# Kernel optimization log

Measured on AMD Instinct MI355X. Metric: run time of the kernel, lower is better.

The kernel has to match this reference:

```python
import jax, jax.numpy as jnp
import numpy as np

DIM = 384
H_RES, W_RES = 56, 56
HEADS = 12
WS = 7          # window size
SS = 3          # shift size
N = WS * WS     # tokens per window
NW = (H_RES // WS) * (W_RES // WS)
EPS = 1e-5


def _rel_pos_index(ws):
    coords = np.stack(np.meshgrid(np.arange(ws), np.arange(ws), indexing='ij'))  # [2,ws,ws]
    cf = coords.reshape(2, -1)                      # [2, N]
    rc = (cf[:, :, None] - cf[:, None, :]).transpose(1, 2, 0)  # [N,N,2]
    rc[..., 0] += ws - 1
    rc[..., 1] += ws - 1
    rc[..., 0] *= 2 * ws - 1
    return rc.sum(-1)                               # [N,N] int


def _attn_mask(h, w, ws, ss):
    img = np.zeros((h, w))
    cnt = 0
    slices = (slice(0, -ws), slice(-ws, -ss), slice(-ss, None))
    for hs in slices:
        for wsl in slices:
            img[hs, wsl] = cnt
            cnt += 1
    mw = img.reshape(h // ws, ws, w // ws, ws).transpose(0, 2, 1, 3).reshape(-1, ws * ws)  # [nW,N]
    d = mw[:, None, :] - mw[:, :, None]
    return np.where(d != 0, -100.0, 0.0).astype(np.float32)  # [nW,N,N]


RPI = jnp.asarray(_rel_pos_index(WS).reshape(-1))          # [N*N]
ATTN_MASK = jnp.asarray(_attn_mask(H_RES, W_RES, WS, SS))  # [nW,N,N]


def _layernorm(x, g, b):
    mu = jnp.mean(x, axis=-1, keepdims=True)
    var = jnp.mean(jnp.square(x - mu), axis=-1, keepdims=True)
    return (x - mu) * jax.lax.rsqrt(var + EPS) * g + b


def setup_inputs() -> dict:
    key = jax.random.key(0)
    ks = jax.random.split(key, 8)
    s = 0.02
    return {
        'x': jax.random.normal(ks[0], (32, 1 + H_RES * W_RES, DIM), jnp.float32),
        'norm1_g': jnp.ones((DIM,), jnp.float32),
        'norm1_b': jnp.zeros((DIM,), jnp.float32),
        'qkv_w': jax.random.normal(ks[1], (DIM, 3 * DIM), jnp.float32) * s,
        'qkv_b': jnp.zeros((3 * DIM,), jnp.float32),
        'rpb_table': jax.random.normal(ks[2], ((2 * WS - 1) ** 2, HEADS), jnp.float32) * s,
        'proj_w': jax.random.normal(ks[3], (DIM, DIM), jnp.float32) * s,
        'proj_b': jnp.zeros((DIM,), jnp.float32),
        'norm2_g': jnp.ones((DIM,), jnp.float32),
        'norm2_b': jnp.zeros((DIM,), jnp.float32),
        'fc1_w': jax.random.normal(ks[4], (DIM, 4 * DIM), jnp.float32) * s,
        'fc1_b': jnp.zeros((4 * DIM,), jnp.float32),
        'fc2_w': jax.random.normal(ks[5], (4 * DIM, DIM), jnp.float32) * s,
        'fc2_b': jnp.zeros((DIM,), jnp.float32),
    }


def reference(x, norm1_g, norm1_b, qkv_w, qkv_b, rpb_table, proj_w, proj_b,
              norm2_g, norm2_b, fc1_w, fc1_b, fc2_w, fc2_b):
    B = x.shape[0]
    C = DIM
    hd = C // HEADS
    scale = hd ** -0.5

    time_token = x[:, :1, :]          # [B,1,C]
    img = x[:, 1:, :]                 # [B,H*W,C]
    shortcut = img

    h = _layernorm(img, norm1_g, norm1_b).reshape(B, H_RES, W_RES, C)
    h = jnp.roll(h, shift=(-SS, -SS), axis=(1, 2))  # cyclic shift

    # window partition -> [B*nW, N, C]
    xw = h.reshape(B, H_RES // WS, WS, W_RES // WS, WS, C)
    xw = xw.transpose(0, 1, 3, 2, 4, 5).reshape(-1, N, C)

    # window attention
    qkv = (xw @ qkv_w + qkv_b).reshape(-1, N, 3, HEADS, hd).transpose(2, 0, 3, 1, 4)
    q, k, v = qkv[0], qkv[1], qkv[2]                 # [B*nW, H, N, hd]
    attn = jnp.einsum('whnd,whmd->whnm', q * scale, k)
    bias = rpb_table[RPI].reshape(N, N, HEADS).transpose(2, 0, 1)  # [H,N,N]
    attn = attn + bias[None]
    attn = attn.reshape(B, NW, HEADS, N, N) + ATTN_MASK[None, :, None]
    attn = jax.nn.softmax(attn.reshape(-1, HEADS, N, N), axis=-1)
    out = jnp.einsum('whnm,whmd->wnhd', attn, v).reshape(-1, N, C)
    out = out @ proj_w + proj_b

    # window reverse -> [B,H,W,C]
    out = out.reshape(B, H_RES // WS, W_RES // WS, WS, WS, C)
    out = out.transpose(0, 1, 3, 2, 4, 5).reshape(B, H_RES, W_RES, C)
    out = jnp.roll(out, shift=(SS, SS), axis=(1, 2)).reshape(B, H_RES * W_RES, C)

    img = shortcut + out
    x = jnp.concatenate([time_token, img], axis=1)   # [B,1+H*W,C]
    x = _layernorm(x, norm2_g, norm2_b)
    hmlp = jax.nn.gelu(x @ fc1_w + fc1_b, approximate=False)
    x = x + (hmlp @ fc2_w + fc2_b)
    return x
```

## Files before the change

### kernel.cpp

```cpp
#include <hip/hip_runtime.h>
#include <hip/hip_bf16.h>

#define DIM 384
#define HEADS 12
#define NTOK 49
#define TOKENS 3137
#define M_ATTN 100352
#define M_FULL 100384
#define M_PAD  100480
#define SCALEQ 0.17677669529663687f

typedef __attribute__((ext_vector_type(8))) short s8v;
typedef __attribute__((ext_vector_type(4))) float f4v;
typedef unsigned short u16;

__device__ __forceinline__ float b2f(int s) {
  union { unsigned u; float f; } c; c.u = ((unsigned)(s & 0xffff)) << 16; return c.f;
}
__device__ __forceinline__ u16 f2b(float f) {
  __hip_bfloat16 h = __float2bfloat16(f);
  return *reinterpret_cast<u16*>(&h);
}
__device__ __forceinline__ void gload16(const void* g, void* l) {
  __builtin_amdgcn_global_load_lds((const __attribute__((address_space(1))) void*)g,
                                   (__attribute__((address_space(3))) void*)l, 16, 0, 0);
}

__global__ void k_convert(const float* __restrict__ qkv_w, const float* __restrict__ qkv_b,
                          const float* __restrict__ proj_w, const float* __restrict__ fc1_w,
                          const float* __restrict__ fc2_w,
                          u16* __restrict__ wt_qkv, float* __restrict__ qkvb_s,
                          u16* __restrict__ wt_proj, u16* __restrict__ wt_fc1,
                          u16* __restrict__ wt_fc2) {
  int i = blockIdx.x * 256 + threadIdx.x;
  if (i < 1152 * 384) { int n = i / 384, k = i % 384;
    float v = qkv_w[(size_t)k * 1152 + n]; if (n < 384) v *= SCALEQ; wt_qkv[i] = f2b(v); }
  if (i < 1152) qkvb_s[i] = qkv_b[i] * (i < 384 ? SCALEQ : 1.0f);
  if (i < 384 * 384) { int n = i / 384, k = i % 384; wt_proj[i] = f2b(proj_w[(size_t)k * 384 + n]); }
  if (i < 1536 * 384) { int n = i / 384, k = i % 384; wt_fc1[i] = f2b(fc1_w[(size_t)k * 1536 + n]); }
  if (i < 384 * 1536) { int n = i / 1536, k = i % 1536; wt_fc2[i] = f2b(fc2_w[(size_t)k * 384 + n]); }
}

__global__ void k_addtab(const float* __restrict__ rpb, float* __restrict__ ADD) {
  int idx = blockIdx.x * 256 + threadIdx.x;
  if (idx >= 4 * HEADS * NTOK * NTOK) return;
  int j = idx % NTOK, t = idx / NTOK;
  int i = t % NTOK; t /= NTOK;
  int h = t % HEADS; int cls = t / HEADS;
  int ii = i / 7, jj = i % 7, ji = j / 7, j2 = j % 7;
  int rpi = (ii - ji + 6) * 13 + (jj - j2 + 6);
  float v = rpb[rpi * HEADS + h];
  int rh = (cls & 2) ? (ii < 4 ? 1 : 2) : 0;
  int rw = (cls & 1) ? (jj < 4 ? 1 : 2) : 0;
  int sh = (cls & 2) ? (ji < 4 ? 1 : 2) : 0;
  int sw = (cls & 1) ? (j2 < 4 ? 1 : 2) : 0;
  if (rh != sh || rw != sw) v -= 100.0f;
  ADD[idx] = v;
}

__global__ void k_ln1(const float* __restrict__ x, const float* __restrict__ g,
                      const float* __restrict__ b, u16* __restrict__ xw, int t0) {
  int wid = threadIdx.x >> 6, lane = threadIdx.x & 63;
  int t = t0 + blockIdx.x * 4 + wid;
  int bi = t / 3136, rem = t % 3136;
  int win = rem / NTOK, n = rem % NTOK;
  int wh = win >> 3, ww = win & 7, ii = n / 7, jj = n % 7;
  int h = (wh * 7 + ii + 3) % 56;
  int w = (ww * 7 + jj + 3) % 56;
  const float* src = x + ((size_t)bi * TOKENS + 1 + h * 56 + w) * DIM;
  float v[6];
  #pragma unroll
  for (int e = 0; e < 6; e++) v[e] = src[lane + e * 64];
  float s = v[0] + v[1] + v[2] + v[3] + v[4] + v[5];
  #pragma unroll
  for (int m = 1; m < 64; m <<= 1) s += __shfl_xor(s, m);
  float mu = s * (1.0f / 384.0f);
  float q = 0.f;
  #pragma unroll
  for (int e = 0; e < 6; e++) { float d = v[e] - mu; q += d * d; }
  #pragma unroll
  for (int m = 1; m < 64; m <<= 1) q += __shfl_xor(q, m);
  float rstd = rsqrtf(q * (1.0f / 384.0f) + 1e-5f);
  u16* dst = xw + (size_t)(t - t0) * DIM;
  #pragma unroll
  for (int e = 0; e < 6; e++) {
    int c = lane + e * 64;
    dst[c] = f2b((v[e] - mu) * rstd * g[c] + b[c]);
  }
}

template<int MODE>
__global__ __launch_bounds__(256) void k_gemm(
    const u16* __restrict__ A, const u16* __restrict__ Bt,
    const float* __restrict__ bias, u16* __restrict__ Cb,
    float* __restrict__ outp, const u16* __restrict__ resid,
    int N, int K, int row_off) {
  __shared__ __align__(16) u16 As[2][128 * 64];
  __shared__ __align__(16) u16 Bs[2][128 * 64];
  int gx = gridDim.x;
  int lid = blockIdx.y * gx + blockIdx.x;
  int nwg = gx * gridDim.y;
  int q = nwg >> 3, r = nwg & 7;
  int xcd = lid & 7, loc = lid >> 3;
  int tile = (xcd < r ? xcd * (q + 1) : r * (q + 1) + (xcd - r) * q) + loc;
  int m0 = (tile / gx) * 128, n0 = (tile % gx) * 128;
  int t = threadIdx.x;
  int lane = t & 63, wave = t >> 6;
  int lo = lane & 15, hi = lane >> 4;
  int wr = (wave >> 1) * 64, wc = (wave & 1) * 64;
  int rl = lane >> 3;
  int sl = (lane & 7) ^ rl;
  const u16* Ag = A + (size_t)(m0 + wave * 32 + rl) * K + sl * 8;
  const u16* Bg = Bt + (size_t)(n0 + wave * 32 + rl) * K + sl * 8;
  f4v acc[4][4];
  #pragma unroll
  for (int m = 0; m < 4; m++)
    #pragma unroll
    for (int n = 0; n < 4; n++) acc[m][n] = (f4v)(0.0f);
  int nt = K >> 6;
#define STAGE(buf, kt) do {                                              \
    u16* al_ = As[buf] + wave * 32 * 64;                                 \
    u16* bl_ = Bs[buf] + wave * 32 * 64;                                 \
    _Pragma("unroll")                                                    \
    for (int g_ = 0; g_ < 4; g_++) {                                     \
      gload16(Ag + (size_t)(g_ * 8) * K + (kt), al_ + g_ * 8 * 64);      \
      gload16(Bg + (size_t)(g_ * 8) * K + (kt), bl_ + g_ * 8 * 64);      \
    } } while (0)
  STAGE(0, 0);
  for (int kt = 0; kt < nt; ++kt) {
    int c = kt & 1;
    if (kt + 1 < nt) {
      STAGE(1 - c, (kt + 1) << 6);
      asm volatile("s_waitcnt vmcnt(8)" ::: "memory");
    } else {
      asm volatile("s_waitcnt vmcnt(0)" ::: "memory");
    }
    __builtin_amdgcn_s_barrier();
    __builtin_amdgcn_sched_barrier(0);
    s8v af[2][4], bfr[2][4];
    #pragma unroll
    for (int kk = 0; kk < 2; kk++) {
      #pragma unroll
      for (int m = 0; m < 4; m++) {
        int row = wr + m * 16 + lo;
        af[kk][m] = *(const s8v*)(As[c] + row * 64 + (((kk * 4 + hi) ^ (row & 7)) * 8));
      }
      #pragma unroll
      for (int n = 0; n < 4; n++) {
        int row = wc + n * 16 + lo;
        bfr[kk][n] = *(const s8v*)(Bs[c] + row * 64 + (((kk * 4 + hi) ^ (row & 7)) * 8));
      }
    }
    asm volatile("s_waitcnt lgkmcnt(0)" ::: "memory");
    __builtin_amdgcn_sched_barrier(0);
    __builtin_amdgcn_s_barrier();
    __builtin_amdgcn_sched_barrier(0);
    __builtin_amdgcn_s_setprio(1);
    #pragma unroll
    for (int kk = 0; kk < 2; kk++)
      #pragma unroll
      for (int m = 0; m < 4; m++)
        #pragma unroll
        for (int n = 0; n < 4; n++)
          acc[m][n] = __builtin_amdgcn_mfma_f32_16x16x32_bf16(af[kk][m], bfr[kk][n], acc[m][n], 0, 0, 0);
    __builtin_amdgcn_s_setprio(0);
  }
#undef STAGE
  #pragma unroll
  for (int m = 0; m < 4; m++) {
    int grow = m0 + wr + m * 16 + hi * 4;
    #pragma unroll
    for (int n = 0; n < 4; n++) {
      int gcol = n0 + wc + n * 16 + lo;
      float bv = bias[gcol];
      #pragma unroll
      for (int r2 = 0; r2 < 4; r2++) {
        float val = acc[m][n][r2] + bv;
        size_t idx = (size_t)(grow + r2) * N + gcol;
        if (MODE == 0) {
          Cb[idx] = f2b(val);
        } else if (MODE == 1) {
          float u = __builtin_fmaf(0.0713548163f * val, val * val, 1.5957691216f * val);
          float gl = val * __builtin_amdgcn_rcpf(1.0f + __expf(-u));
          Cb[idx] = f2b(gl);
        } else {
          int orow = grow + r2 + row_off;
          if (orow < M_FULL) {
            size_t oi = (size_t)orow * DIM + gcol;
            outp[oi] = val + b2f(resid[oi]);
          }
        }
      }
    }
  }
}

__global__ __launch_bounds__(256) void k_attn2(const u16* __restrict__ qkv,
                                               const float* __restrict__ ADD,
                                               u16* __restrict__ ao, int win0) {
  __shared__ u16 PT[4][64][76];
  __shared__ u16 VT[4][32][76];
  int wid = threadIdx.x >> 6, lane = threadIdx.x & 63;
  int lo = lane & 15, hi = lane >> 4;
  int win_l = blockIdx.x * 4 + wid;
  int nw = (win0 + win_l) & 63;
  int wh = nw >> 3, ww = nw & 7;
  int cls = ((wh == 7) ? 2 : 0) + ((ww == 7) ? 1 : 0);
  size_t rowbase = (size_t)win_l * NTOK;
  u16 (*pt)[76] = PT[wid];
  u16 (*vt)[76] = VT[wid];

  int rcl[4];
  #pragma unroll
  for (int ti = 0; ti < 4; ti++) {
    int r = ti * 16 + lo;
    rcl[ti] = r < NTOK ? r : NTOK - 1;
  }
  int jrow = lane < NTOK ? lane : NTOK - 1;

  for (int h = 0; h < HEADS; h++) {
    s8v af[4], bf[4];
    #pragma unroll
    for (int ti = 0; ti < 4; ti++) {
      af[ti] = *(const s8v*)(qkv + (rowbase + rcl[ti]) * 1152 + h * 32 + hi * 8);
      bf[ti] = *(const s8v*)(qkv + (rowbase + rcl[ti]) * 1152 + 384 + h * 32 + hi * 8);
    }
    f4v st[4][4];
    #pragma unroll
    for (int mi = 0; mi < 4; mi++)
      #pragma unroll
      for (int ni = 0; ni < 4; ni++)
        st[mi][ni] = __builtin_amdgcn_mfma_f32_16x16x32_bf16(af[mi], bf[ni], (f4v)(0.0f), 0, 0, 0);

    {
      const u16* vsrc = qkv + (rowbase + jrow) * 1152 + 768 + h * 32;
      #pragma unroll
      for (int d0 = 0; d0 < 32; d0 += 8) {
        s8v v = *(const s8v*)(vsrc + d0);
        #pragma unroll
        for (int e = 0; e < 8; e++) vt[d0 + e][lane] = (u16)v[e];
      }
    }

    const float* addb = ADD + ((size_t)cls * HEADS + h) * (NTOK * NTOK);
    #pragma unroll
    for (int mi = 0; mi < 4; mi++)
      #pragma unroll
      for (int ni = 0; ni < 4; ni++) {
        int jj = ni * 16 + lo;
        #pragma unroll
        for (int r = 0; r < 4; r++) {
          int i = mi * 16 + hi * 4 + r;
          if (jj < NTOK) {
            int ic = i < NTOK ? i : NTOK - 1;
            st[mi][ni][r] += addb[ic * NTOK + jj];
          } else st[mi][ni][r] = -1e30f;
        }
      }

    float invl[4][4];
    #pragma unroll
    for (int mi = 0; mi < 4; mi++)
      #pragma unroll
      for (int r = 0; r < 4; r++) {
        float m = fmaxf(fmaxf(st[mi][0][r], st[mi][1][r]), fmaxf(st[mi][2][r], st[mi][3][r]));
        #pragma unroll
        for (int msk = 1; msk < 16; msk <<= 1) m = fmaxf(m, __shfl_xor(m, msk));
        float s = 0.f;
        #pragma unroll
        for (int ni = 0; ni < 4; ni++) {
          float p = __expf(st[mi][ni][r] - m);
          st[mi][ni][r] = p;
          s += p;
        }
        #pragma unroll
        for (int msk = 1; msk < 16; msk <<= 1) s += __shfl_xor(s, msk);
        invl[mi][r] = 1.0f / s;
      }

    #pragma unroll
    for (int ni = 0; ni < 4; ni++)
      #pragma unroll
      for (int mi = 0; mi < 4; mi++) {
        ushort4 pk;
        pk.x = f2b(st[mi][ni][0]); pk.y = f2b(st[mi][ni][1]);
        pk.z = f2b(st[mi][ni][2]); pk.w = f2b(st[mi][ni][3]);
        *(ushort4*)(&pt[ni * 16 + lo][mi * 16 + hi * 4]) = pk;
      }

    f4v ot[4][2];
    #pragma unroll
    for (int mi = 0; mi < 4; mi++)
      #pragma unroll
      for (int dt = 0; dt < 2; dt++) ot[mi][dt] = (f4v)(0.0f);
    #pragma unroll
    for (int kt = 0; kt < 2; kt++) {
      s8v pa[4], vb[2];
      #pragma unroll
      for (int mi = 0; mi < 4; mi++) {
        s8v p;
        #pragma unroll
        for (int e = 0; e < 8; e++) p[e] = (short)pt[kt * 32 + hi * 8 + e][mi * 16 + lo];
        pa[mi] = p;
      }
      #pragma unroll
      for (int dt = 0; dt < 2; dt++) {
        short4 a = *(const short4*)(&vt[dt * 16 + lo][kt * 32 + hi * 8]);
        short4 b = *(const short4*)(&vt[dt * 16 + lo][kt * 32 + hi * 8 + 4]);
        s8v v; v[0] = a.x; v[1] = a.y; v[2] = a.z; v[3] = a.w;
               v[4] = b.x; v[5] = b.y; v[6] = b.z; v[7] = b.w;
        vb[dt] = v;
      }
      #pragma unroll
      for (int mi = 0; mi < 4; mi++)
        #pragma unroll
        for (int dt = 0; dt < 2; dt++)
          ot[mi][dt] = __builtin_amdgcn_mfma_f32_16x16x32_bf16(pa[mi], vb[dt], ot[mi][dt], 0, 0, 0);
    }

    #pragma unroll
    for (int mi = 0; mi < 4; mi++)
      #pragma unroll
      for (int r = 0; r < 4; r++) {
        int i = mi * 16 + hi * 4 + r;
        if (i < NTOK) {
          u16* op = ao + (rowbase + i) * DIM + h * 32 + lo;
          op[0]  = f2b(ot[mi][0][r] * invl[mi][r]);
          op[16] = f2b(ot[mi][1][r] * invl[mi][r]);
        }
      }
  }
}

__global__ void k_ln2(const float* __restrict__ x, const u16* __restrict__ proj,
                      const float* __restrict__ g, const float* __restrict__ b,
                      u16* __restrict__ x2b) {
  int wid = threadIdx.x >> 6, lane = threadIdx.x & 63;
  int r = blockIdx.x * 4 + wid;
  u16* dst = x2b + (size_t)r * DIM;
  if (r >= M_FULL) {
    u16 z = f2b(0.0f);
    #pragma unroll
    for (int e = 0; e < 6; e++) dst[lane + e * 64] = z;
    return;
  }
  int bi = r / TOKENS, tk = r % TOKENS;
  const float* xs = x + (size_t)r * DIM;
  float v[6];
  if (tk == 0) {
    #pragma unroll
    for (int e = 0; e < 6; e++) v[e] = xs[lane + e * 64];
  } else {
    int p = tk - 1, hh = p / 56, wp = p % 56;
    int a = (hh + 53) % 56, bw = (wp + 53) % 56;
    int wh = a / 7, ii = a % 7, w2 = bw / 7, jj = bw % 7;
    size_t prow = ((size_t)bi * 64 + wh * 8 + w2) * NTOK + ii * 7 + jj;
    const u16* ps = proj + prow * DIM;
    #pragma unroll
    for (int e = 0; e < 6; e++) v[e] = xs[lane + e * 64] + b2f(ps[lane + e * 64]);
  }
  float s = v[0] + v[1] + v[2] + v[3] + v[4] + v[5];
  #pragma unroll
  for (int m = 1; m < 64; m <<= 1) s += __shfl_xor(s, m);
  float mu = s * (1.0f / 384.0f);
  float q = 0.f;
  #pragma unroll
  for (int e = 0; e < 6; e++) { float d = v[e] - mu; q += d * d; }
  #pragma unroll
  for (int m = 1; m < 64; m <<= 1) q += __shfl_xor(q, m);
  float rstd = rsqrtf(q * (1.0f / 384.0f) + 1e-5f);
  #pragma unroll
  for (int e = 0; e < 6; e++) {
    int c = lane + e * 64;
    dst[c] = f2b((v[e] - mu) * rstd * g[c] + b[c]);
  }
}

extern "C" void kernel_launch(void* const* d_in, const int* in_sizes, int n_in,
                              void* d_out, int out_size, void* d_ws, size_t ws_size,
                              hipStream_t stream) {
  const float* x      = (const float*)d_in[0];
  const float* n1g    = (const float*)d_in[1];
  const float* n1b    = (const float*)d_in[2];
  const float* qkv_w  = (const float*)d_in[3];
  const float* qkv_b  = (const float*)d_in[4];
  const float* rpb    = (const float*)d_in[5];
  const float* proj_w = (const float*)d_in[6];
  const float* proj_b = (const float*)d_in[7];
  const float* n2g    = (const float*)d_in[8];
  const float* n2b    = (const float*)d_in[9];
  const float* fc1_w  = (const float*)d_in[10];
  const float* fc1_b  = (const float*)d_in[11];
  const float* fc2_w  = (const float*)d_in[12];
  const float* fc2_b  = (const float*)d_in[13];
  float* outp = (float*)d_out;

  auto al = [](size_t v) { return (v + 255) & ~(size_t)255; };
  const int cand[8][2] = {{1,1},{1,2},{2,2},{2,4},{4,4},{4,8},{8,8},{16,16}};
  int NC1 = 16, NC2 = 16;
  for (int ci = 0; ci < 8; ci++) {
    int c1 = cand[ci][0], c2 = cand[ci][1];
    int cbb = (785 + c2 - 1) / c2;
    size_t tot = al(884736) + al(294912) + al(1179648) + al(1179648) + al(4608)
               + al(460992)
               + al((size_t)(M_ATTN / c1) * 768)
               + al((size_t)(M_ATTN / c1) * 2304)
               + al((size_t)M_ATTN * 768)
               + al((size_t)M_PAD * 768)
               + al((size_t)cbb * 128 * 1536 * 2);
    if (tot <= ws_size) { NC1 = c1; NC2 = c2; break; }
  }
  char* p = (char*)d_ws;
  auto take = [&](size_t bytes) { char* r = p; p += al(bytes); return r; };
  u16* wt_qkv  = (u16*)take(884736);
  u16* wt_proj = (u16*)take(294912);
  u16* wt_fc1  = (u16*)take(1179648);
  u16* wt_fc2  = (u16*)take(1179648);
  float* qkvb_s = (float*)take(4608);
  float* ADDt   = (float*)take(460992);
  int chunkM = M_ATTN / NC1;
  u16* XW   = (u16*)take((size_t)chunkM * 768);
  u16* QKV  = (u16*)take((size_t)chunkM * 2304);
  u16* PROJ = (u16*)take((size_t)M_ATTN * 768);
  u16* X2B  = (u16*)take((size_t)M_PAD * 768);
  int cb = (785 + NC2 - 1) / NC2;
  u16* FC1  = (u16*)take((size_t)cb * 128 * 1536 * 2);
  u16* AO = XW;

  k_convert<<<2304, 256, 0, stream>>>(qkv_w, qkv_b, proj_w, fc1_w, fc2_w,
                                      wt_qkv, qkvb_s, wt_proj, wt_fc1, wt_fc2);
  k_addtab<<<451, 256, 0, stream>>>(rpb, ADDt);
  int chunkWin = chunkM / NTOK;
  for (int c = 0; c < NC1; c++) {
    int t0 = c * chunkM;
    k_ln1<<<chunkM / 4, 256, 0, stream>>>(x, n1g, n1b, XW, t0);
    k_gemm<0><<<dim3(9, chunkM / 128), 256, 0, stream>>>(XW, wt_qkv, qkvb_s, QKV,
                                                         nullptr, nullptr, 1152, 384, 0);
    k_attn2<<<chunkWin / 4, 256, 0, stream>>>(QKV, ADDt, AO, c * chunkWin);
    k_gemm<0><<<dim3(3, chunkM / 128), 256, 0, stream>>>(AO, wt_proj, proj_b,
                                                         PROJ + (size_t)t0 * DIM,
                                                         nullptr, nullptr, 384, 384, 0);
  }
  k_ln2<<<M_PAD / 4, 256, 0, stream>>>(x, PROJ, n2g, n2b, X2B);
  for (int c = 0; c < NC2; c++) {
    int rb0 = c * cb;
    int nb = 785 - rb0; if (nb > cb) nb = cb; if (nb <= 0) break;
    k_gemm<1><<<dim3(12, nb), 256, 0, stream>>>(X2B + (size_t)rb0 * 128 * DIM, wt_fc1,
                                                fc1_b, FC1, nullptr, nullptr, 1536, 384, 0);
    k_gemm<2><<<dim3(3, nb), 256, 0, stream>>>(FC1, wt_fc2, fc2_b, nullptr, outp, X2B,
                                               384, 1536, rb0 * 128);
  }
}
```

Measured before the change: 1.007 ms.

## Store GEMM operands in pre-tiled swizzled layout and split attention per head

GEMM operands (weights, LN outputs, attention output, FC1 activations) are now written by their producers into a tile-contiguous, XOR-swizzled 128x64 layout. Each GEMM stage can then load a tile as contiguous 16-byte chunks instead of strided row segments. The attention kernel now assigns one wave per (window, head) instead of looping over 12 heads per wave, which raises parallelism. The workspace is reorganised so the PROJ and FC1 buffers share one region, and the chunk candidates start at 4, trading more scattered producer stores for cheaper GEMM loads.

```diff
diff --git a/kernel.cpp b/kernel.cpp
--- a/kernel.cpp
+++ b/kernel.cpp
@@ -25,6 +25,14 @@
   __builtin_amdgcn_global_load_lds((const __attribute__((address_space(1))) void*)g,
                                    (__attribute__((address_space(3))) void*)l, 16, 0, 0);
 }
+__device__ __forceinline__ float gelu_f(float val) {
+  float u = __builtin_fmaf(0.0713548163f * val, val * val, 1.5957691216f * val);
+  return val * __builtin_amdgcn_rcpf(1.0f + __expf(-u));
+}
+__device__ __forceinline__ size_t tidx(int tile, int KS, int rl, int c) {
+  return ((size_t)(tile * KS + (c >> 6)) * 128 + rl) * 64
+       + (((((c >> 3) & 7)) ^ (rl & 7)) << 3) + (c & 7);
+}
 
 __global__ void k_convert(const float* __restrict__ qkv_w, const float* __restrict__ qkv_b,
                           const float* __restrict__ proj_w, const float* __restrict__ fc1_w,
@@ -34,11 +42,15 @@
                           u16* __restrict__ wt_fc2) {
   int i = blockIdx.x * 256 + threadIdx.x;
   if (i < 1152 * 384) { int n = i / 384, k = i % 384;
-    float v = qkv_w[(size_t)k * 1152 + n]; if (n < 384) v *= SCALEQ; wt_qkv[i] = f2b(v); }
+    float v = qkv_w[(size_t)k * 1152 + n]; if (n < 384) v *= SCALEQ;
+    wt_qkv[tidx(n >> 7, 6, n & 127, k)] = f2b(v); }
   if (i < 1152) qkvb_s[i] = qkv_b[i] * (i < 384 ? SCALEQ : 1.0f);
-  if (i < 384 * 384) { int n = i / 384, k = i % 384; wt_proj[i] = f2b(proj_w[(size_t)k * 384 + n]); }
-  if (i < 1536 * 384) { int n = i / 384, k = i % 384; wt_fc1[i] = f2b(fc1_w[(size_t)k * 1536 + n]); }
-  if (i < 384 * 1536) { int n = i / 1536, k = i % 1536; wt_fc2[i] = f2b(fc2_w[(size_t)k * 384 + n]); }
+  if (i < 384 * 384) { int n = i / 384, k = i % 384;
+    wt_proj[tidx(n >> 7, 6, n & 127, k)] = f2b(proj_w[(size_t)k * 384 + n]); }
+  if (i < 1536 * 384) { int n = i / 384, k = i % 384;
+    wt_fc1[tidx(n >> 7, 6, n & 127, k)] = f2b(fc1_w[(size_t)k * 1536 + n]); }
+  if (i < 384 * 1536) { int n = i / 1536, k = i % 1536;
+    wt_fc2[tidx(n >> 7, 24, n & 127, k)] = f2b(fc2_w[(size_t)k * 384 + n]); }
 }
 
 __global__ void k_addtab(const float* __restrict__ rpb, float* __restrict__ ADD) {
@@ -59,9 +71,10 @@
 }
 
 __global__ void k_ln1(const float* __restrict__ x, const float* __restrict__ g,
-                      const float* __restrict__ b, u16* __restrict__ xw, int t0) {
+                      const float* __restrict__ b, u16* __restrict__ xwt, int t0) {
   int wid = threadIdx.x >> 6, lane = threadIdx.x & 63;
-  int t = t0 + blockIdx.x * 4 + wid;
+  int ml = blockIdx.x * 4 + wid;
+  int t = t0 + ml;
   int bi = t / 3136, rem = t % 3136;
   int win = rem / NTOK, n = rem % NTOK;
   int wh = win >> 3, ww = win & 7, ii = n / 7, jj = n % 7;
@@ -81,20 +94,20 @@
   #pragma unroll
   for (int m = 1; m < 64; m <<= 1) q += __shfl_xor(q, m);
   float rstd = rsqrtf(q * (1.0f / 384.0f) + 1e-5f);
-  u16* dst = xw + (size_t)(t - t0) * DIM;
+  int tile = ml >> 7, rl = ml & 127;
   #pragma unroll
   for (int e = 0; e < 6; e++) {
     int c = lane + e * 64;
-    dst[c] = f2b((v[e] - mu) * rstd * g[c] + b[c]);
+    xwt[tidx(tile, 6, rl, c)] = f2b((v[e] - mu) * rstd * g[c] + b[c]);
   }
 }
 
 template<int MODE>
 __global__ __launch_bounds__(256) void k_gemm(
-    const u16* __restrict__ A, const u16* __restrict__ Bt,
+    const u16* __restrict__ At, const u16* __restrict__ Bt,
     const float* __restrict__ bias, u16* __restrict__ Cb,
-    float* __restrict__ outp, const u16* __restrict__ resid,
-    int N, int K, int row_off) {
+    float* __restrict__ outp, const u16* __restrict__ residt,
+    int N, int KT, int row_off) {
   __shared__ __align__(16) u16 As[2][128 * 64];
   __shared__ __align__(16) u16 Bs[2][128 * 64];
   int gx = gridDim.x;
@@ -108,29 +121,26 @@
   int lane = t & 63, wave = t >> 6;
   int lo = lane & 15, hi = lane >> 4;
   int wr = (wave >> 1) * 64, wc = (wave & 1) * 64;
-  int rl = lane >> 3;
-  int sl = (lane & 7) ^ rl;
-  const u16* Ag = A + (size_t)(m0 + wave * 32 + rl) * K + sl * 8;
-  const u16* Bg = Bt + (size_t)(n0 + wave * 32 + rl) * K + sl * 8;
+  const u16* Ag = At + ((size_t)(m0 >> 7) * KT) * 8192 + wave * 2048 + lane * 8;
+  const u16* Bg = Bt + ((size_t)(n0 >> 7) * KT) * 8192 + wave * 2048 + lane * 8;
   f4v acc[4][4];
   #pragma unroll
   for (int m = 0; m < 4; m++)
     #pragma unroll
     for (int n = 0; n < 4; n++) acc[m][n] = (f4v)(0.0f);
-  int nt = K >> 6;
 #define STAGE(buf, kt) do {                                              \
-    u16* al_ = As[buf] + wave * 32 * 64;                                 \
-    u16* bl_ = Bs[buf] + wave * 32 * 64;                                 \
+    u16* al_ = As[buf] + wave * 2048;                                    \
+    u16* bl_ = Bs[buf] + wave * 2048;                                    \
     _Pragma("unroll")                                                    \
     for (int g_ = 0; g_ < 4; g_++) {                                     \
-      gload16(Ag + (size_t)(g_ * 8) * K + (kt), al_ + g_ * 8 * 64);      \
-      gload16(Bg + (size_t)(g_ * 8) * K + (kt), bl_ + g_ * 8 * 64);      \
+      gload16(Ag + (size_t)(kt) * 8192 + g_ * 512, al_ + g_ * 512);      \
+      gload16(Bg + (size_t)(kt) * 8192 + g_ * 512, bl_ + g_ * 512);      \
     } } while (0)
   STAGE(0, 0);
-  for (int kt = 0; kt < nt; ++kt) {
+  for (int kt = 0; kt < KT; ++kt) {
     int c = kt & 1;
-    if (kt + 1 < nt) {
-      STAGE(1 - c, (kt + 1) << 6);
+    if (kt + 1 < KT) {
+      STAGE(1 - c, kt + 1);
       asm volatile("s_waitcnt vmcnt(8)" ::: "memory");
     } else {
       asm volatile("s_waitcnt vmcnt(0)" ::: "memory");
@@ -168,26 +178,23 @@
 #undef STAGE
   #pragma unroll
   for (int m = 0; m < 4; m++) {
-    int grow = m0 + wr + m * 16 + hi * 4;
     #pragma unroll
     for (int n = 0; n < 4; n++) {
       int gcol = n0 + wc + n * 16 + lo;
       float bv = bias[gcol];
       #pragma unroll
       for (int r2 = 0; r2 < 4; r2++) {
+        int lrow = wr + m * 16 + hi * 4 + r2;
         float val = acc[m][n][r2] + bv;
-        size_t idx = (size_t)(grow + r2) * N + gcol;
         if (MODE == 0) {
-          Cb[idx] = f2b(val);
+          Cb[(size_t)(m0 + lrow) * N + gcol] = f2b(val);
         } else if (MODE == 1) {
-          float u = __builtin_fmaf(0.0713548163f * val, val * val, 1.5957691216f * val);
-          float gl = val * __builtin_amdgcn_rcpf(1.0f + __expf(-u));
-          Cb[idx] = f2b(gl);
+          Cb[tidx(m0 >> 7, 24, lrow, gcol)] = f2b(gelu_f(val));
         } else {
-          int orow = grow + r2 + row_off;
+          int orow = m0 + lrow + row_off;
           if (orow < M_FULL) {
-            size_t oi = (size_t)orow * DIM + gcol;
-            outp[oi] = val + b2f(resid[oi]);
+            float res = b2f(residt[tidx(orow >> 7, 6, orow & 127, gcol)]);
+            outp[(size_t)orow * 384 + gcol] = val + res;
           }
         }
       }
@@ -197,12 +204,13 @@
 
 __global__ __launch_bounds__(256) void k_attn2(const u16* __restrict__ qkv,
                                                const float* __restrict__ ADD,
-                                               u16* __restrict__ ao, int win0) {
+                                               u16* __restrict__ aot, int win0) {
   __shared__ u16 PT[4][64][76];
   __shared__ u16 VT[4][32][76];
   int wid = threadIdx.x >> 6, lane = threadIdx.x & 63;
   int lo = lane & 15, hi = lane >> 4;
-  int win_l = blockIdx.x * 4 + wid;
+  int gw = blockIdx.x * 4 + wid;
+  int win_l = gw / HEADS, h = gw % HEADS;
   int nw = (win0 + win_l) & 63;
   int wh = nw >> 3, ww = nw & 7;
   int cls = ((wh == 7) ? 2 : 0) + ((ww == 7) ? 1 : 0);
@@ -218,130 +226,129 @@
   }
   int jrow = lane < NTOK ? lane : NTOK - 1;
 
-  for (int h = 0; h < HEADS; h++) {
-    s8v af[4], bf[4];
-    #pragma unroll
-    for (int ti = 0; ti < 4; ti++) {
-      af[ti] = *(const s8v*)(qkv + (rowbase + rcl[ti]) * 1152 + h * 32 + hi * 8);
-      bf[ti] = *(const s8v*)(qkv + (rowbase + rcl[ti]) * 1152 + 384 + h * 32 + hi * 8);
-    }
-    f4v st[4][4];
-    #pragma unroll
-    for (int mi = 0; mi < 4; mi++)
-      #pragma unroll
-      for (int ni = 0; ni < 4; ni++)
-        st[mi][ni] = __builtin_amdgcn_mfma_f32_16x16x32_bf16(af[mi], bf[ni], (f4v)(0.0f), 0, 0, 0);
-
-    {
-      const u16* vsrc = qkv + (rowbase + jrow) * 1152 + 768 + h * 32;
-      #pragma unroll
-      for (int d0 = 0; d0 < 32; d0 += 8) {
-        s8v v = *(const s8v*)(vsrc + d0);
-        #pragma unroll
-        for (int e = 0; e < 8; e++) vt[d0 + e][lane] = (u16)v[e];
-      }
-    }
-
-    const float* addb = ADD + ((size_t)cls * HEADS + h) * (NTOK * NTOK);
-    #pragma unroll
-    for (int mi = 0; mi < 4; mi++)
-      #pragma unroll
-      for (int ni = 0; ni < 4; ni++) {
-        int jj = ni * 16 + lo;
-        #pragma unroll
-        for (int r = 0; r < 4; r++) {
-          int i = mi * 16 + hi * 4 + r;
-          if (jj < NTOK) {
-            int ic = i < NTOK ? i : NTOK - 1;
-            st[mi][ni][r] += addb[ic * NTOK + jj];
-          } else st[mi][ni][r] = -1e30f;
-        }
-      }
-
-    float invl[4][4];
-    #pragma unroll
-    for (int mi = 0; mi < 4; mi++)
-      #pragma unroll
-      for (int r = 0; r < 4; r++) {
-        float m = fmaxf(fmaxf(st[mi][0][r], st[mi][1][r]), fmaxf(st[mi][2][r], st[mi][3][r]));
-        #pragma unroll
-        for (int msk = 1; msk < 16; msk <<= 1) m = fmaxf(m, __shfl_xor(m, msk));
-        float s = 0.f;
-        #pragma unroll
-        for (int ni = 0; ni < 4; ni++) {
-          float p = __expf(st[mi][ni][r] - m);
-          st[mi][ni][r] = p;
-          s += p;
-        }
-        #pragma unroll
-        for (int msk = 1; msk < 16; msk <<= 1) s += __shfl_xor(s, msk);
-        invl[mi][r] = 1.0f / s;
-      }
-
+  s8v af[4], bf[4];
+  #pragma unroll
+  for (int ti = 0; ti < 4; ti++) {
+    af[ti] = *(const s8v*)(qkv + (rowbase + rcl[ti]) * 1152 + h * 32 + hi * 8);
+    bf[ti] = *(const s8v*)(qkv + (rowbase + rcl[ti]) * 1152 + 384 + h * 32 + hi * 8);
+  }
+  f4v st[4][4];
+  #pragma unroll
+  for (int mi = 0; mi < 4; mi++)
     #pragma unroll
     for (int ni = 0; ni < 4; ni++)
-      #pragma unroll
-      for (int mi = 0; mi < 4; mi++) {
-        ushort4 pk;
-        pk.x = f2b(st[mi][ni][0]); pk.y = f2b(st[mi][ni][1]);
-        pk.z = f2b(st[mi][ni][2]); pk.w = f2b(st[mi][ni][3]);
-        *(ushort4*)(&pt[ni * 16 + lo][mi * 16 + hi * 4]) = pk;
-      }
-
-    f4v ot[4][2];
-    #pragma unroll
-    for (int mi = 0; mi < 4; mi++)
-      #pragma unroll
-      for (int dt = 0; dt < 2; dt++) ot[mi][dt] = (f4v)(0.0f);
-    #pragma unroll
-    for (int kt = 0; kt < 2; kt++) {
-      s8v pa[4], vb[2];
-      #pragma unroll
-      for (int mi = 0; mi < 4; mi++) {
-        s8v p;
-        #pragma unroll
-        for (int e = 0; e < 8; e++) p[e] = (short)pt[kt * 32 + hi * 8 + e][mi * 16 + lo];
-        pa[mi] = p;
-      }
-      #pragma unroll
-      for (int dt = 0; dt < 2; dt++) {
-        short4 a = *(const short4*)(&vt[dt * 16 + lo][kt * 32 + hi * 8]);
-        short4 b = *(const short4*)(&vt[dt * 16 + lo][kt * 32 + hi * 8 + 4]);
-        s8v v; v[0] = a.x; v[1] = a.y; v[2] = a.z; v[3] = a.w;
-               v[4] = b.x; v[5] = b.y; v[6] = b.z; v[7] = b.w;
-        vb[dt] = v;
-      }
-      #pragma unroll
-      for (int mi = 0; mi < 4; mi++)
-        #pragma unroll
-        for (int dt = 0; dt < 2; dt++)
-          ot[mi][dt] = __builtin_amdgcn_mfma_f32_16x16x32_bf16(pa[mi], vb[dt], ot[mi][dt], 0, 0, 0);
-    }
-
-    #pragma unroll
-    for (int mi = 0; mi < 4; mi++)
+      st[mi][ni] = __builtin_amdgcn_mfma_f32_16x16x32_bf16(af[mi], bf[ni], (f4v)(0.0f), 0, 0, 0);
+
+  {
+    const u16* vsrc = qkv + (rowbase + jrow) * 1152 + 768 + h * 32;
+    #pragma unroll
+    for (int d0 = 0; d0 < 32; d0 += 8) {
+      s8v v = *(const s8v*)(vsrc + d0);
+      #pragma unroll
+      for (int e = 0; e < 8; e++) vt[d0 + e][lane] = (u16)v[e];
+    }
+  }
+
+  const float* addb = ADD + ((size_t)cls * HEADS + h) * (NTOK * NTOK);
+  #pragma unroll
+  for (int mi = 0; mi < 4; mi++)
+    #pragma unroll
+    for (int ni = 0; ni < 4; ni++) {
+      int jj = ni * 16 + lo;
       #pragma unroll
       for (int r = 0; r < 4; r++) {
         int i = mi * 16 + hi * 4 + r;
-        if (i < NTOK) {
-          u16* op = ao + (rowbase + i) * DIM + h * 32 + lo;
-          op[0]  = f2b(ot[mi][0][r] * invl[mi][r]);
-          op[16] = f2b(ot[mi][1][r] * invl[mi][r]);
-        }
-      }
-  }
+        if (jj < NTOK) {
+          int ic = i < NTOK ? i : NTOK - 1;
+          st[mi][ni][r] += addb[ic * NTOK + jj];
+        } else st[mi][ni][r] = -1e30f;
+      }
+    }
+
+  float invl[4][4];
+  #pragma unroll
+  for (int mi = 0; mi < 4; mi++)
+    #pragma unroll
+    for (int r = 0; r < 4; r++) {
+      float m = fmaxf(fmaxf(st[mi][0][r], st[mi][1][r]), fmaxf(st[mi][2][r], st[mi][3][r]));
+      #pragma unroll
+      for (int msk = 1; msk < 16; msk <<= 1) m = fmaxf(m, __shfl_xor(m, msk));
+      float s = 0.f;
+      #pragma unroll
+      for (int ni = 0; ni < 4; ni++) {
+        float p = __expf(st[mi][ni][r] - m);
+        st[mi][ni][r] = p;
+        s += p;
+      }
+      #pragma unroll
+      for (int msk = 1; msk < 16; msk <<= 1) s += __shfl_xor(s, msk);
+      invl[mi][r] = 1.0f / s;
+    }
+
+  #pragma unroll
+  for (int ni = 0; ni < 4; ni++)
+    #pragma unroll
+    for (int mi = 0; mi < 4; mi++) {
+      ushort4 pk;
+      pk.x = f2b(st[mi][ni][0]); pk.y = f2b(st[mi][ni][1]);
+      pk.z = f2b(st[mi][ni][2]); pk.w = f2b(st[mi][ni][3]);
+      *(ushort4*)(&pt[ni * 16 + lo][mi * 16 + hi * 4]) = pk;
+    }
+
+  f4v ot[4][2];
+  #pragma unroll
+  for (int mi = 0; mi < 4; mi++)
+    #pragma unroll
+    for (int dt = 0; dt < 2; dt++) ot[mi][dt] = (f4v)(0.0f);
+  #pragma unroll
+  for (int kt = 0; kt < 2; kt++) {
+    s8v pa[4], vb[2];
+    #pragma unroll
+    for (int mi = 0; mi < 4; mi++) {
+      s8v p;
+      #pragma unroll
+      for (int e = 0; e < 8; e++) p[e] = (short)pt[kt * 32 + hi * 8 + e][mi * 16 + lo];
+      pa[mi] = p;
+    }
+    #pragma unroll
+    for (int dt = 0; dt < 2; dt++) {
+      short4 a = *(const short4*)(&vt[dt * 16 + lo][kt * 32 + hi * 8]);
+      short4 b = *(const short4*)(&vt[dt * 16 + lo][kt * 32 + hi * 8 + 4]);
+      s8v v; v[0] = a.x; v[1] = a.y; v[2] = a.z; v[3] = a.w;
+             v[4] = b.x; v[5] = b.y; v[6] = b.z; v[7] = b.w;
+      vb[dt] = v;
+    }
+    #pragma unroll
+    for (int mi = 0; mi < 4; mi++)
+      #pragma unroll
+      for (int dt = 0; dt < 2; dt++)
+        ot[mi][dt] = __builtin_amdgcn_mfma_f32_16x16x32_bf16(pa[mi], vb[dt], ot[mi][dt], 0, 0, 0);
+  }
+
+  #pragma unroll
+  for (int mi = 0; mi < 4; mi++)
+    #pragma unroll
+    for (int r = 0; r < 4; r++) {
+      int i = mi * 16 + hi * 4 + r;
+      if (i < NTOK) {
+        int row = (int)rowbase + i;
+        int tile = row >> 7, rl = row & 127;
+        aot[tidx(tile, 6, rl, h * 32 + lo)]      = f2b(ot[mi][0][r] * invl[mi][r]);
+        aot[tidx(tile, 6, rl, h * 32 + 16 + lo)] = f2b(ot[mi][1][r] * invl[mi][r]);
+      }
+    }
 }
 
 __global__ void k_ln2(const float* __restrict__ x, const u16* __restrict__ proj,
                       const float* __restrict__ g, const float* __restrict__ b,
-                      u16* __restrict__ x2b) {
+                      u16* __restrict__ x2bt) {
   int wid = threadIdx.x >> 6, lane = threadIdx.x & 63;
   int r = blockIdx.x * 4 + wid;
-  u16* dst = x2b + (size_t)r * DIM;
+  int tile = r >> 7, rl = r & 127;
   if (r >= M_FULL) {
     u16 z = f2b(0.0f);
     #pragma unroll
-    for (int e = 0; e < 6; e++) dst[lane + e * 64] = z;
+    for (int e = 0; e < 6; e++) x2bt[tidx(tile, 6, rl, lane + e * 64)] = z;
     return;
   }
   int bi = r / TOKENS, tk = r % TOKENS;
@@ -372,7 +379,7 @@
   #pragma unroll
   for (int e = 0; e < 6; e++) {
     int c = lane + e * 64;
-    dst[c] = f2b((v[e] - mu) * rstd * g[c] + b[c]);
+    x2bt[tidx(tile, 6, rl, c)] = f2b((v[e] - mu) * rstd * g[c] + b[c]);
   }
 }
 
@@ -396,18 +403,18 @@
   float* outp = (float*)d_out;
 
   auto al = [](size_t v) { return (v + 255) & ~(size_t)255; };
-  const int cand[8][2] = {{1,1},{1,2},{2,2},{2,4},{4,4},{4,8},{8,8},{16,16}};
+  size_t base = al(884736) + al(294912) + al(1179648) + al(1179648) + al(4608)
+              + al(460992) + al((size_t)M_PAD * 768);
+  const int cand[3][2] = {{4, 4}, {8, 8}, {16, 16}};
   int NC1 = 16, NC2 = 16;
-  for (int ci = 0; ci < 8; ci++) {
+  for (int ci = 0; ci < 3; ci++) {
     int c1 = cand[ci][0], c2 = cand[ci][1];
-    int cbb = (785 + c2 - 1) / c2;
-    size_t tot = al(884736) + al(294912) + al(1179648) + al(1179648) + al(4608)
-               + al(460992)
-               + al((size_t)(M_ATTN / c1) * 768)
-               + al((size_t)(M_ATTN / c1) * 2304)
-               + al((size_t)M_ATTN * 768)
-               + al((size_t)M_PAD * 768)
-               + al((size_t)cbb * 128 * 1536 * 2);
+    size_t cm = M_ATTN / c1;
+    size_t cb_ = (785 + c2 - 1) / c2;
+    size_t region = (size_t)M_ATTN * 768;
+    size_t fc1b = cb_ * 24 * 8192 * 2;
+    if (fc1b > region) region = fc1b;
+    size_t tot = base + 2 * al(cm * 768) + al(cm * 2304) + al(region);
     if (tot <= ws_size) { NC1 = c1; NC2 = c2; break; }
   }
   char* p = (char*)d_ws;
@@ -418,14 +425,17 @@
   u16* wt_fc2  = (u16*)take(1179648);
   float* qkvb_s = (float*)take(4608);
   float* ADDt   = (float*)take(460992);
+  u16* X2Bt = (u16*)take((size_t)M_PAD * 768);
   int chunkM = M_ATTN / NC1;
-  u16* XW   = (u16*)take((size_t)chunkM * 768);
+  u16* XWt  = (u16*)take((size_t)chunkM * 768);
   u16* QKV  = (u16*)take((size_t)chunkM * 2304);
-  u16* PROJ = (u16*)take((size_t)M_ATTN * 768);
-  u16* X2B  = (u16*)take((size_t)M_PAD * 768);
+  u16* AOt  = (u16*)take((size_t)chunkM * 768);
   int cb = (785 + NC2 - 1) / NC2;
-  u16* FC1  = (u16*)take((size_t)cb * 128 * 1536 * 2);
-  u16* AO = XW;
+  size_t region = (size_t)M_ATTN * 768;
+  size_t fc1b = (size_t)cb * 24 * 8192 * 2;
+  if (fc1b > region) region = fc1b;
+  u16* PROJ = (u16*)take(region);
+  u16* FC1t = PROJ;
 
   k_convert<<<2304, 256, 0, stream>>>(qkv_w, qkv_b, proj_w, fc1_w, fc2_w,
                                       wt_qkv, qkvb_s, wt_proj, wt_fc1, wt_fc2);
@@ -433,21 +443,21 @@
   int chunkWin = chunkM / NTOK;
   for (int c = 0; c < NC1; c++) {
     int t0 = c * chunkM;
-    k_ln1<<<chunkM / 4, 256, 0, stream>>>(x, n1g, n1b, XW, t0);
-    k_gemm<0><<<dim3(9, chunkM / 128), 256, 0, stream>>>(XW, wt_qkv, qkvb_s, QKV,
-                                                         nullptr, nullptr, 1152, 384, 0);
-    k_attn2<<<chunkWin / 4, 256, 0, stream>>>(QKV, ADDt, AO, c * chunkWin);
-    k_gemm<0><<<dim3(3, chunkM / 128), 256, 0, stream>>>(AO, wt_proj, proj_b,
+    k_ln1<<<chunkM / 4, 256, 0, stream>>>(x, n1g, n1b, XWt, t0);
+    k_gemm<0><<<dim3(9, chunkM / 128), 256, 0, stream>>>(XWt, wt_qkv, qkvb_s, QKV,
+                                                         nullptr, nullptr, 1152, 6, 0);
+    k_attn2<<<chunkWin * HEADS / 4, 256, 0, stream>>>(QKV, ADDt, AOt, c * chunkWin);
+    k_gemm<0><<<dim3(3, chunkM / 128), 256, 0, stream>>>(AOt, wt_proj, proj_b,
                                                          PROJ + (size_t)t0 * DIM,
-                                                         nullptr, nullptr, 384, 384, 0);
-  }
-  k_ln2<<<M_PAD / 4, 256, 0, stream>>>(x, PROJ, n2g, n2b, X2B);
+                                                         nullptr, nullptr, 384, 6, 0);
+  }
+  k_ln2<<<M_PAD / 4, 256, 0, stream>>>(x, PROJ, n2g, n2b, X2Bt);
   for (int c = 0; c < NC2; c++) {
     int rb0 = c * cb;
     int nb = 785 - rb0; if (nb > cb) nb = cb; if (nb <= 0) break;
-    k_gemm<1><<<dim3(12, nb), 256, 0, stream>>>(X2B + (size_t)rb0 * 128 * DIM, wt_fc1,
-                                                fc1_b, FC1, nullptr, nullptr, 1536, 384, 0);
-    k_gemm<2><<<dim3(3, nb), 256, 0, stream>>>(FC1, wt_fc2, fc2_b, nullptr, outp, X2B,
-                                               384, 1536, rb0 * 128);
-  }
-}
+    k_gemm<1><<<dim3(12, nb), 256, 0, stream>>>(X2Bt + (size_t)rb0 * 128 * 384, wt_fc1,
+                                                fc1_b, FC1t, nullptr, nullptr, 1536, 6, 0);
+    k_gemm<2><<<dim3(3, nb), 256, 0, stream>>>(FC1t, wt_fc2, fc2_b, nullptr, outp, X2Bt,
+                                               384, 24, rb0 * 128);
+  }
+}
```

Measured after the change: 1.048 ms. 4.0% more time.
